# Optimization experiments

Hardware: AMD Instinct MI355X
Metric: run time of the kernel (lower is better)

The kernel has to match this reference:

```python
import jax, jax.numpy as jnp
import numpy as np

H = 512                      # hidden_dim
C, T, F = 2, 128, 257        # output_dims
FLAT = C * T * F             # 65792 flattened spectrogram frame
CD, SD = 256, 256            # content_dim, style_dim
D_IN = CD + SD + FLAT        # GRU input size


def setup_inputs() -> dict:
    key = jax.random.key(0)
    ks = jax.random.split(key, 8)
    B, S = 4, 16
    sc = 0.02  # small init so tanh/sigmoid stay in a sane range
    return {
        "content_emb": jax.random.normal(ks[0], (B, S, CD), jnp.float32),
        "style_emb": jax.random.normal(ks[1], (B, SD), jnp.float32),
        "start_token": jax.random.normal(ks[2], (FLAT,), jnp.float32),
        "W_ih": jax.random.normal(ks[3], (3 * H, D_IN), jnp.float32) * sc,
        "W_hh": jax.random.normal(ks[4], (3 * H, H), jnp.float32) * sc,
        "b_ih": jnp.zeros((3 * H,), jnp.float32),
        "b_hh": jnp.zeros((3 * H,), jnp.float32),
        "W_proj": jax.random.normal(ks[5], (FLAT, H), jnp.float32) * sc,
        "b_proj": jnp.zeros((FLAT,), jnp.float32),
    }


def _gru_cell(x, h, W_ih, W_hh, b_ih, b_hh):
    # PyTorch GRU gate order: r, z, n
    gi = x @ W_ih.T + b_ih          # (B, 3H)
    gh = h @ W_hh.T + b_hh          # (B, 3H)
    i_r, i_z, i_n = jnp.split(gi, 3, axis=-1)
    h_r, h_z, h_n = jnp.split(gh, 3, axis=-1)
    r = jax.nn.sigmoid(i_r + h_r)
    z = jax.nn.sigmoid(i_z + h_z)
    n = jnp.tanh(i_n + r * h_n)
    return (1.0 - z) * n + z * h


def reference(content_emb, style_emb, start_token, W_ih, W_hh, b_ih, b_hh, W_proj, b_proj):
    B, S, _ = content_emb.shape
    h0 = jnp.zeros((B, H), content_emb.dtype)
    prev0 = jnp.broadcast_to(start_token, (B, FLAT))

    def step(carry, c_s):
        h, prev = carry
        # concat [content_s, style, prev_output] -> (B, D_IN)
        x = jnp.concatenate([c_s, style_emb, prev], axis=-1)
        h = _gru_cell(x, h, W_ih, W_hh, b_ih, b_hh)
        out = h @ W_proj.T + b_proj   # (B, FLAT)
        return (h, out), out

    _, outs = jax.lax.scan(step, (h0, prev0), jnp.swapaxes(content_emb, 0, 1))
    outs = jnp.swapaxes(outs, 0, 1)   # (B, S, FLAT)
    return outs.reshape(B, S, C, T, F)
```

## Files before the change

kernel.cpp:

```cpp
#include <hip/hip_runtime.h>
#include <hip/hip_bf16.h>
#include <math.h>

typedef __bf16 bf16x8 __attribute__((ext_vector_type(8)));
typedef float  f32x4  __attribute__((ext_vector_type(4)));

#define HDIM   512
#define FLAT   65792
#define DIN    66304
#define G3     1536
#define NSLAB  2056
#define MS     512
#define KSPLIT 21
#define CHUNK  98

#define BH_BYTES   67371008ULL
#define MBUF_BYTES  3145728ULL
#define BP_BYTES       6144ULL
#define ST_BYTES       6144ULL
#define GIB_BYTES    393216ULL
#define HALL_BYTES   131072ULL
#define HBF_BYTES     65536ULL

__device__ __forceinline__ ushort f2bf(float f) {
    uint u = __float_as_uint(f);
    u += 0x7FFFu + ((u >> 16) & 1u);
    return (ushort)(u >> 16);
}
__device__ __forceinline__ uint pk2(float a, float b) {
    return (uint)f2bf(a) | ((uint)f2bf(b) << 16);
}

__global__ __launch_bounds__(256) void buildBh(const float* __restrict__ Wp,
                                               ushort* __restrict__ Bh) {
    const int s    = blockIdx.x;
    const int lane = threadIdx.x & 63;
    const int wave = threadIdx.x >> 6;
    const int lrow = lane & 15;
    const int quad = lane >> 4;
    const float* base = Wp + (size_t)s * 32 * 512;
    ushort* out = Bh + (size_t)s * 16384;
#pragma unroll
    for (int i = 0; i < 8; ++i) {
        const int t = wave + i * 4;
        const int col = t * 16 + lrow;
        float v[8];
#pragma unroll
        for (int j = 0; j < 8; ++j)
            v[j] = base[(size_t)(quad * 8 + j) * 512 + col];
        uint4 pr;
        pr.x = pk2(v[0], v[1]);
        pr.y = pk2(v[2], v[3]);
        pr.z = pk2(v[4], v[5]);
        pr.w = pk2(v[6], v[7]);
        *(uint4*)(out + (size_t)t * 512 + (size_t)lane * 8) = pr;
    }
}

__global__ __launch_bounds__(512, 2) void gemmM(const float* __restrict__ Wih,
                                                const ushort* __restrict__ Bh,
                                                const float* __restrict__ bproj,
                                                const float* __restrict__ start,
                                                float* __restrict__ Mbuf,
                                                float* __restrict__ bpA,
                                                float* __restrict__ stA) {
    const int tid  = threadIdx.x;
    const int lane = tid & 63;
    const int wave = tid >> 6;
    const int mg   = wave >> 2;
    const int ng   = wave & 3;
    const int lrow = lane & 15;
    const int quad = lane >> 4;
    const int mtile = blockIdx.x % 12;
    const int kc    = blockIdx.x / 12;
    const int s0 = kc * CHUNK;
    const int s1 = min(s0 + CHUNK, NSLAB);

    const int rowBase = mtile * 128 + mg * 64 + lrow;
    const float* aP[4];
#pragma unroll
    for (int mf = 0; mf < 4; ++mf)
        aP[mf] = Wih + (size_t)(rowBase + mf * 16) * DIN + 512 + quad * 8;
    const ushort* bBase = Bh + (size_t)(ng * 8) * 512 + (size_t)lane * 8;

    f32x4 acc[4][8];
#pragma unroll
    for (int mf = 0; mf < 4; ++mf)
#pragma unroll
        for (int nf = 0; nf < 8; ++nf) acc[mf][nf] = (f32x4){0.f, 0.f, 0.f, 0.f};
    float bpAcc[4] = {0.f, 0.f, 0.f, 0.f};
    float stAcc[4] = {0.f, 0.f, 0.f, 0.f};

    float4 a0[4], a1[4];
#pragma unroll
    for (int mf = 0; mf < 4; ++mf) {
        a0[mf] = *(const float4*)(aP[mf] + (size_t)s0 * 32);
        a1[mf] = *(const float4*)(aP[mf] + (size_t)s0 * 32 + 4);
    }

    for (int s = s0; s < s1; ++s) {
        uint4 bReg[8];
        const ushort* bs = bBase + (size_t)s * 16384;
#pragma unroll
        for (int nf = 0; nf < 8; ++nf)
            bReg[nf] = *(const uint4*)(bs + nf * 512);
        if (ng == 0) {
            const float4 bp0 = *(const float4*)(bproj + s * 32 + quad * 8);
            const float4 bp1 = *(const float4*)(bproj + s * 32 + quad * 8 + 4);
            const float4 st0 = *(const float4*)(start + s * 32 + quad * 8);
            const float4 st1 = *(const float4*)(start + s * 32 + quad * 8 + 4);
#pragma unroll
            for (int mf = 0; mf < 4; ++mf) {
                bpAcc[mf] += a0[mf].x * bp0.x + a0[mf].y * bp0.y + a0[mf].z * bp0.z + a0[mf].w * bp0.w
                           + a1[mf].x * bp1.x + a1[mf].y * bp1.y + a1[mf].z * bp1.z + a1[mf].w * bp1.w;
                stAcc[mf] += a0[mf].x * st0.x + a0[mf].y * st0.y + a0[mf].z * st0.z + a0[mf].w * st0.w
                           + a1[mf].x * st1.x + a1[mf].y * st1.y + a1[mf].z * st1.z + a1[mf].w * st1.w;
            }
        }
        bf16x8 af[4];
#pragma unroll
        for (int mf = 0; mf < 4; ++mf) {
            uint4 pr;
            pr.x = pk2(a0[mf].x, a0[mf].y);
            pr.y = pk2(a0[mf].z, a0[mf].w);
            pr.z = pk2(a1[mf].x, a1[mf].y);
            pr.w = pk2(a1[mf].z, a1[mf].w);
            af[mf] = __builtin_bit_cast(bf16x8, pr);
        }
        if (s + 1 < s1) {
#pragma unroll
            for (int mf = 0; mf < 4; ++mf) {
                a0[mf] = *(const float4*)(aP[mf] + (size_t)(s + 1) * 32);
                a1[mf] = *(const float4*)(aP[mf] + (size_t)(s + 1) * 32 + 4);
            }
        }
#pragma unroll
        for (int nf = 0; nf < 8; ++nf) {
            const bf16x8 bf = __builtin_bit_cast(bf16x8, bReg[nf]);
#pragma unroll
            for (int mf = 0; mf < 4; ++mf)
                acc[mf][nf] = __builtin_amdgcn_mfma_f32_16x16x32_bf16(af[mf], bf, acc[mf][nf], 0, 0, 0);
        }
    }
#pragma unroll
    for (int mf = 0; mf < 4; ++mf)
#pragma unroll
        for (int nf = 0; nf < 8; ++nf) {
            const int col = (ng * 8 + nf) * 16 + lrow;
#pragma unroll
            for (int r = 0; r < 4; ++r) {
                const int row = mtile * 128 + mg * 64 + mf * 16 + quad * 4 + r;
                atomicAdd(&Mbuf[(size_t)row * MS + col], acc[mf][nf][r]);
            }
        }
    if (ng == 0) {
#pragma unroll
        for (int mf = 0; mf < 4; ++mf) {
            float bp = bpAcc[mf], st = stAcc[mf];
            bp += __shfl_xor(bp, 16); bp += __shfl_xor(bp, 32);
            st += __shfl_xor(st, 16); st += __shfl_xor(st, 32);
            if (lane < 16) {
                atomicAdd(&bpA[rowBase + mf * 16], bp);
                atomicAdd(&stA[rowBase + mf * 16], st);
            }
        }
    }
}

__global__ __launch_bounds__(256) void giBase(const float* __restrict__ Wih,
                                              const float* __restrict__ content,
                                              const float* __restrict__ style,
                                              const float* __restrict__ bih,
                                              const float* __restrict__ bpA,
                                              const float* __restrict__ stA,
                                              float* __restrict__ giB) {
    const int j = (blockIdx.x * blockDim.x + threadIdx.x) >> 6;
    if (j >= G3) return;
    const int lane = threadIdx.x & 63;
    const int b = lane >> 4;
    const int s = lane & 15;
    const float* wr = Wih + (size_t)j * DIN;
    const float* cp = content + (size_t)lane * 256;
    const float* sp = style + (size_t)b * 256;
    float acc = 0.f;
#pragma unroll 4
    for (int d = 0; d < 256; d += 4) {
        const float4 w = *(const float4*)(wr + d);
        const float4 x = *(const float4*)(cp + d);
        acc += w.x * x.x + w.y * x.y + w.z * x.z + w.w * x.w;
    }
#pragma unroll 4
    for (int d = 0; d < 256; d += 4) {
        const float4 w = *(const float4*)(wr + 256 + d);
        const float4 x = *(const float4*)(sp + d);
        acc += w.x * x.x + w.y * x.y + w.z * x.z + w.w * x.w;
    }
    acc += bih[j] + ((s == 0) ? stA[j] : bpA[j]);
    giB[(size_t)lane * G3 + j] = acc;
}

__global__ __launch_bounds__(256) void stepK(const float* __restrict__ Mbuf,
                                             const float* __restrict__ Whh,
                                             const float* __restrict__ bhh,
                                             const float* __restrict__ giB,
                                             float* __restrict__ hAll,
                                             ushort* __restrict__ hBf,
                                             const int s) {
    const int gw   = (blockIdx.x * blockDim.x + threadIdx.x) >> 6;
    const int lane = threadIdx.x & 63;
    const int b = gw & 3;
    const int j = gw >> 2;
    float dMr = 0.f, dMz = 0.f, dMn = 0.f, dWr = 0.f, dWz = 0.f, dWn = 0.f;
    if (s > 0) {
        const float* h = hAll + (size_t)((s - 1) * 4 + b) * HDIM;
        float hr[8];
#pragma unroll
        for (int i = 0; i < 8; ++i) hr[i] = h[i * 64 + lane];
        const float* M0 = Mbuf + (size_t)j * MS;
        const float* M1 = Mbuf + (size_t)(j + 512) * MS;
        const float* M2 = Mbuf + (size_t)(j + 1024) * MS;
        const float* W0 = Whh + (size_t)j * HDIM;
        const float* W1 = Whh + (size_t)(j + 512) * HDIM;
        const float* W2 = Whh + (size_t)(j + 1024) * HDIM;
#pragma unroll
        for (int i = 0; i < 8; ++i) {
            const int d = i * 64 + lane;
            dMr += M0[d] * hr[i]; dMz += M1[d] * hr[i]; dMn += M2[d] * hr[i];
            dWr += W0[d] * hr[i]; dWz += W1[d] * hr[i]; dWn += W2[d] * hr[i];
        }
#pragma unroll
        for (int m = 1; m < 64; m <<= 1) {
            dMr += __shfl_xor(dMr, m); dMz += __shfl_xor(dMz, m); dMn += __shfl_xor(dMn, m);
            dWr += __shfl_xor(dWr, m); dWz += __shfl_xor(dWz, m); dWn += __shfl_xor(dWn, m);
        }
    }
    if (lane == 0) {
        const float* gb = giB + (size_t)(b * 16 + s) * G3;
        const float gir = gb[j] + dMr;
        const float giz = gb[j + 512] + dMz;
        const float gin = gb[j + 1024] + dMn;
        const float ghr = bhh[j] + dWr;
        const float ghz = bhh[j + 512] + dWz;
        const float ghn = bhh[j + 1024] + dWn;
        const float r = 1.f / (1.f + expf(-(gir + ghr)));
        const float z = 1.f / (1.f + expf(-(giz + ghz)));
        const float n = tanhf(gin + r * ghn);
        const float hp = (s > 0) ? hAll[(size_t)((s - 1) * 4 + b) * HDIM + j] : 0.f;
        const float hn = (1.f - z) * n + z * hp;
        hAll[(size_t)(s * 4 + b) * HDIM + j] = hn;
        hBf[(size_t)(s * 4 + b) * HDIM + j] = f2bf(hn);
    }
}

__global__ __launch_bounds__(256) void projK(const float* __restrict__ Wp,
                                             const float* __restrict__ bproj,
                                             const ushort* __restrict__ hBf,
                                             float* __restrict__ out) {
    const int lane = threadIdx.x & 63;
    const int wave = threadIdx.x >> 6;
    const int f0   = blockIdx.x * 256 + wave * 64;
    const int lrow = lane & 15;
    const int quad = lane >> 4;
    f32x4 acc[4][4];
#pragma unroll
    for (int pt = 0; pt < 4; ++pt)
#pragma unroll
        for (int ft = 0; ft < 4; ++ft) acc[pt][ft] = (f32x4){0.f, 0.f, 0.f, 0.f};

    for (int d0 = 0; d0 < HDIM; d0 += 32) {
        bf16x8 afr[4];
#pragma unroll
        for (int pt = 0; pt < 4; ++pt)
            afr[pt] = __builtin_bit_cast(bf16x8,
                *(const uint4*)(hBf + (size_t)(pt * 16 + lrow) * HDIM + d0 + quad * 8));
#pragma unroll
        for (int ft = 0; ft < 4; ++ft) {
            const float* wrow = Wp + (size_t)(f0 + ft * 16 + lrow) * HDIM + d0 + quad * 8;
            const float4 w0 = *(const float4*)(wrow);
            const float4 w1 = *(const float4*)(wrow + 4);
            uint4 pr;
            pr.x = pk2(w0.x, w0.y);
            pr.y = pk2(w0.z, w0.w);
            pr.z = pk2(w1.x, w1.y);
            pr.w = pk2(w1.z, w1.w);
            const bf16x8 bfr = __builtin_bit_cast(bf16x8, pr);
#pragma unroll
            for (int pt = 0; pt < 4; ++pt)
                acc[pt][ft] = __builtin_amdgcn_mfma_f32_16x16x32_bf16(afr[pt], bfr, acc[pt][ft], 0, 0, 0);
        }
    }
#pragma unroll
    for (int pt = 0; pt < 4; ++pt)
#pragma unroll
        for (int ft = 0; ft < 4; ++ft) {
            const int f = f0 + ft * 16 + lrow;
            const float bp = bproj[f];
#pragma unroll
            for (int r = 0; r < 4; ++r) {
                const int p = pt * 16 + quad * 4 + r;
                const int ss = p >> 2;
                const int bb = p & 3;
                out[(size_t)(bb * 16 + ss) * FLAT + f] = acc[pt][ft][r] + bp;
            }
        }
}

extern "C" void kernel_launch(void* const* d_in, const int* in_sizes, int n_in,
                              void* d_out, int out_size, void* d_ws, size_t ws_size,
                              hipStream_t stream) {
    const float* content = (const float*)d_in[0];
    const float* style   = (const float*)d_in[1];
    const float* start   = (const float*)d_in[2];
    const float* Wih     = (const float*)d_in[3];
    const float* Whh     = (const float*)d_in[4];
    const float* bih     = (const float*)d_in[5];
    const float* bhh     = (const float*)d_in[6];
    const float* Wproj   = (const float*)d_in[7];
    const float* bproj   = (const float*)d_in[8];
    float* out = (float*)d_out;

    char* ws = (char*)d_ws;
    ushort* Bh   = (ushort*)(ws);
    float*  Mbuf = (float*)(ws + BH_BYTES);
    float*  bpA  = (float*)(ws + BH_BYTES + MBUF_BYTES);
    float*  stA  = (float*)(ws + BH_BYTES + MBUF_BYTES + BP_BYTES);
    float*  giB  = (float*)(ws + BH_BYTES + MBUF_BYTES + BP_BYTES + ST_BYTES);
    float*  hAll = (float*)(ws + BH_BYTES + MBUF_BYTES + BP_BYTES + ST_BYTES + GIB_BYTES);
    ushort* hBf  = (ushort*)(ws + BH_BYTES + MBUF_BYTES + BP_BYTES + ST_BYTES + GIB_BYTES + HALL_BYTES);

    hipMemsetAsync(Mbuf, 0, MBUF_BYTES + BP_BYTES + ST_BYTES, stream);
    buildBh<<<NSLAB, 256, 0, stream>>>(Wproj, Bh);
    gemmM<<<12 * KSPLIT, 512, 0, stream>>>(Wih, Bh, bproj, start, Mbuf, bpA, stA);
    giBase<<<384, 256, 0, stream>>>(Wih, content, style, bih, bpA, stA, giB);
    for (int s = 0; s < 16; ++s)
        stepK<<<512, 256, 0, stream>>>(Mbuf, Whh, bhh, giB, hAll, hBf, s);
    projK<<<FLAT / 256, 256, 0, stream>>>(Wproj, bproj, hBf, out);
}
```

Measured before the change: 1.030 ms.

## Stage B slabs into double-buffered LDS via direct global-to-LDS loads

```diff
diff --git a/kernel.cpp b/kernel.cpp
--- a/kernel.cpp
+++ b/kernel.cpp
@@ -64,6 +64,7 @@
                                                 float* __restrict__ Mbuf,
                                                 float* __restrict__ bpA,
                                                 float* __restrict__ stA) {
+    __shared__ ushort Blds[2 * 16384];
     const int tid  = threadIdx.x;
     const int lane = tid & 63;
     const int wave = tid >> 6;
@@ -81,7 +82,8 @@
 #pragma unroll
     for (int mf = 0; mf < 4; ++mf)
         aP[mf] = Wih + (size_t)(rowBase + mf * 16) * DIN + 512 + quad * 8;
-    const ushort* bBase = Bh + (size_t)(ng * 8) * 512 + (size_t)lane * 8;
+
+    const char* gStage = (const char*)Bh + (size_t)(wave * 4) * 1024 + (size_t)lane * 16;
 
     f32x4 acc[4][8];
 #pragma unroll
@@ -91,19 +93,34 @@
     float bpAcc[4] = {0.f, 0.f, 0.f, 0.f};
     float stAcc[4] = {0.f, 0.f, 0.f, 0.f};
 
+#pragma unroll
+    for (int i = 0; i < 4; ++i) {
+        __builtin_amdgcn_global_load_lds(
+            (const __attribute__((address_space(1))) uint*)(gStage + (size_t)s0 * 32768 + i * 1024),
+            (__attribute__((address_space(3))) uint*)(Blds + (size_t)(wave * 4 + i) * 512),
+            16, 0, 0);
+    }
     float4 a0[4], a1[4];
 #pragma unroll
     for (int mf = 0; mf < 4; ++mf) {
         a0[mf] = *(const float4*)(aP[mf] + (size_t)s0 * 32);
         a1[mf] = *(const float4*)(aP[mf] + (size_t)s0 * 32 + 4);
     }
+    __syncthreads();
 
     for (int s = s0; s < s1; ++s) {
-        uint4 bReg[8];
-        const ushort* bs = bBase + (size_t)s * 16384;
-#pragma unroll
-        for (int nf = 0; nf < 8; ++nf)
-            bReg[nf] = *(const uint4*)(bs + nf * 512);
+        const int cur = (s - s0) & 1;
+        if (s + 1 < s1) {
+            const char* gs = gStage + (size_t)(s + 1) * 32768;
+            ushort* ld = Blds + (size_t)(cur ^ 1) * 16384 + (size_t)(wave * 4) * 512;
+#pragma unroll
+            for (int i = 0; i < 4; ++i) {
+                __builtin_amdgcn_global_load_lds(
+                    (const __attribute__((address_space(1))) uint*)(gs + i * 1024),
+                    (__attribute__((address_space(3))) uint*)(ld + i * 512),
+                    16, 0, 0);
+            }
+        }
         if (ng == 0) {
             const float4 bp0 = *(const float4*)(bproj + s * 32 + quad * 8);
             const float4 bp1 = *(const float4*)(bproj + s * 32 + quad * 8 + 4);
@@ -134,13 +151,15 @@
                 a1[mf] = *(const float4*)(aP[mf] + (size_t)(s + 1) * 32 + 4);
             }
         }
+        const ushort* bBuf = Blds + (size_t)cur * 16384 + (size_t)(ng * 8) * 512 + (size_t)lane * 8;
 #pragma unroll
         for (int nf = 0; nf < 8; ++nf) {
-            const bf16x8 bf = __builtin_bit_cast(bf16x8, bReg[nf]);
+            const bf16x8 bf = __builtin_bit_cast(bf16x8, *(const uint4*)(bBuf + nf * 512));
 #pragma unroll
             for (int mf = 0; mf < 4; ++mf)
                 acc[mf][nf] = __builtin_amdgcn_mfma_f32_16x16x32_bf16(af[mf], bf, acc[mf][nf], 0, 0, 0);
         }
+        __syncthreads();
     }
 #pragma unroll
     for (int mf = 0; mf < 4; ++mf)
```

New measurement: 1.053 ms. +2.3%, slower.
